# Kernel optimization log

Measured on AMD Instinct MI355X. Metric: run time of the kernel, lower is better.

The kernel has to match this reference:

```python
import jax, jax.numpy as jnp
import numpy as np


def setup_inputs() -> dict:
    key = jax.random.key(0)
    k1, k2 = jax.random.split(key)
    B, La, Lb, D = 32, 512, 512, 768
    a_bar = jax.random.normal(k1, (B, La, D), dtype=jnp.float32)
    b_bar = jax.random.normal(k2, (B, Lb, D), dtype=jnp.float32)
    return {"a_bar": a_bar, "b_bar": b_bar}


def reference(a_bar, b_bar):
    # e: [B, La, Lb] cross-attention scores
    e = jnp.einsum('bad,bcd->bac', a_bar, b_bar)
    # attend over b positions (softmax dim=2) -> aligned representation of a
    a_tilde = jnp.einsum('bac,bcd->bad', jax.nn.softmax(e, axis=2), b_bar)
    # attend over a positions (softmax dim=1), transpose, bmm with a_bar
    b_tilde = jnp.einsum('bac,bad->bcd', jax.nn.softmax(e, axis=1), a_bar)
    m_a = jnp.concatenate([a_bar, a_tilde, a_bar - a_tilde, a_bar * a_tilde], axis=-1)
    m_b = jnp.concatenate([b_bar, b_tilde, b_bar - b_tilde, b_bar * b_tilde], axis=-1)
    return (m_a, m_b)
```

## Files before the change

kernel.cpp:

```cpp
#include <hip/hip_runtime.h>
#include <hip/hip_bf16.h>
#include <math.h>

#define NB 32
#define LA 512
#define LB 512
#define DD 768

typedef __bf16 bf16x4 __attribute__((ext_vector_type(4)));
typedef __bf16 bf16x8 __attribute__((ext_vector_type(8)));
typedef float f32x4 __attribute__((ext_vector_type(4)));

#define LSTR 40

__device__ __forceinline__ void gload_lds16(const void* g, void* l) {
  __builtin_amdgcn_global_load_lds(
      (const __attribute__((address_space(1))) unsigned int*)g,
      (__attribute__((address_space(3))) unsigned int*)l, 16, 0, 0);
}

__global__ __launch_bounds__(256) void convert_kernel(
    const float* __restrict__ A, const float* __restrict__ B,
    __bf16* __restrict__ Ah, __bf16* __restrict__ Al,
    __bf16* __restrict__ Bh, __bf16* __restrict__ Bl,
    __bf16* __restrict__ AhT, __bf16* __restrict__ BhT) {
  const int zb = blockIdx.z;
  const int b = zb & (NB - 1);
  const bool isB = zb >= NB;
  const float* src = (isB ? B : A) + (size_t)b * 512 * DD;
  __bf16* H = (isB ? Bh : Ah) + (size_t)b * 512 * DD;
  __bf16* L = (isB ? Bl : Al) + (size_t)b * 512 * DD;
  __bf16* T = (isB ? BhT : AhT) + (size_t)b * DD * 512;
  const int d0 = blockIdx.x * 64, i0 = blockIdx.y * 64;
  __shared__ __bf16 Tt[64][72];
  const int t = threadIdx.x;
  const int c4 = t & 15, r = t >> 4;
#pragma unroll
  for (int p = 0; p < 4; ++p) {
    const int i = i0 + r + p * 16;
    const float4 v = *(const float4*)(src + (size_t)i * DD + d0 + c4 * 4);
    float vv[4] = {v.x, v.y, v.z, v.w};
    bf16x4 h, l;
#pragma unroll
    for (int q = 0; q < 4; ++q) {
      h[q] = (__bf16)vv[q];
      l[q] = (__bf16)(vv[q] - (float)h[q]);
    }
    *(bf16x4*)(H + (size_t)i * DD + d0 + c4 * 4) = h;
    *(bf16x4*)(L + (size_t)i * DD + d0 + c4 * 4) = l;
#pragma unroll
    for (int q = 0; q < 4; ++q) Tt[c4 * 4 + q][r + p * 16] = h[q];
  }
  __syncthreads();
  const int cc = t & 7, rr = t >> 3;
#pragma unroll
  for (int p = 0; p < 2; ++p) {
    const int d = d0 + rr + p * 32;
    *(bf16x8*)(T + (size_t)d * 512 + i0 + cc * 8) =
        *(bf16x8*)&Tt[rr + p * 32][cc * 8];
  }
}

__global__ __launch_bounds__(256) void gemm_e_mfma(
    const __bf16* __restrict__ Ah, const __bf16* __restrict__ Al,
    const __bf16* __restrict__ Bh, const __bf16* __restrict__ Bl,
    float* __restrict__ E) {
  __shared__ __bf16 AhS[128][32], AlS[128][32], BhS[128][32], BlS[128][32];

  const int b = blockIdx.z;
  const int i0 = blockIdx.x * 128, j0 = blockIdx.y * 128;
  const __bf16* AhB = Ah + (size_t)b * LA * DD;
  const __bf16* AlB = Al + (size_t)b * LA * DD;
  const __bf16* BhB = Bh + (size_t)b * LB * DD;
  const __bf16* BlB = Bl + (size_t)b * LB * DD;
  float* Eb = E + (size_t)b * LA * LB;

  const int t = threadIdx.x;
  const int lane = t & 63, wave = t >> 6;
  const int wm = (wave >> 1) * 64, wn = (wave & 1) * 64;
  const int quad = lane >> 4, l16 = lane & 15;
  const int lrow = lane >> 2, lcol = (lane & 3) * 8;

  f32x4 acc[4][4] = {};

  for (int k0 = 0; k0 < DD; k0 += 32) {
    __syncthreads();
#pragma unroll
    for (int n = 0; n < 2; ++n) {
      const int c = n * 4 + wave;
      const int row = c * 16 + lrow;
      const size_t gA = (size_t)(i0 + row) * DD + k0 + lcol;
      const size_t gB = (size_t)(j0 + row) * DD + k0 + lcol;
      gload_lds16(AhB + gA, (char*)&AhS[0][0] + c * 1024);
      gload_lds16(AlB + gA, (char*)&AlS[0][0] + c * 1024);
      gload_lds16(BhB + gB, (char*)&BhS[0][0] + c * 1024);
      gload_lds16(BlB + gB, (char*)&BlS[0][0] + c * 1024);
    }
    __syncthreads();

    bf16x8 fah[4], fal[4], fbh[4], fbl[4];
#pragma unroll
    for (int f = 0; f < 4; ++f) {
      fah[f] = *(bf16x8*)&AhS[wm + f * 16 + l16][quad * 8];
      fal[f] = *(bf16x8*)&AlS[wm + f * 16 + l16][quad * 8];
      fbh[f] = *(bf16x8*)&BhS[wn + f * 16 + l16][quad * 8];
      fbl[f] = *(bf16x8*)&BlS[wn + f * 16 + l16][quad * 8];
    }
#pragma unroll
    for (int fm = 0; fm < 4; ++fm)
#pragma unroll
      for (int fn = 0; fn < 4; ++fn) {
        acc[fm][fn] = __builtin_amdgcn_mfma_f32_16x16x32_bf16(fah[fm], fbh[fn], acc[fm][fn], 0, 0, 0);
        acc[fm][fn] = __builtin_amdgcn_mfma_f32_16x16x32_bf16(fah[fm], fbl[fn], acc[fm][fn], 0, 0, 0);
        acc[fm][fn] = __builtin_amdgcn_mfma_f32_16x16x32_bf16(fal[fm], fbh[fn], acc[fm][fn], 0, 0, 0);
      }
  }

#pragma unroll
  for (int fm = 0; fm < 4; ++fm)
#pragma unroll
    for (int r = 0; r < 4; ++r) {
      const int i = i0 + wm + fm * 16 + quad * 4 + r;
#pragma unroll
      for (int fn = 0; fn < 4; ++fn)
        Eb[(size_t)i * LB + j0 + wn + fn * 16 + l16] = acc[fm][fn][r];
    }
}

__global__ __launch_bounds__(256) void row_stats_kernel(
    const float* __restrict__ E, float* __restrict__ rmax,
    float* __restrict__ rsum) {
  const int wave = threadIdx.x >> 6;
  const int lane = threadIdx.x & 63;
  const int row = blockIdx.x * 4 + wave;
  const float* Er = E + (size_t)row * LB;
  float vals[8];
  float m = -INFINITY;
#pragma unroll
  for (int c = 0; c < 8; ++c) {
    vals[c] = Er[lane + c * 64];
    m = fmaxf(m, vals[c]);
  }
#pragma unroll
  for (int off = 32; off > 0; off >>= 1) m = fmaxf(m, __shfl_xor(m, off));
  float s = 0.f;
#pragma unroll
  for (int c = 0; c < 8; ++c) s += __expf(vals[c] - m);
#pragma unroll
  for (int off = 32; off > 0; off >>= 1) s += __shfl_xor(s, off);
  if (lane == 0) { rmax[row] = m; rsum[row] = s; }
}

__global__ __launch_bounds__(256) void col_partial(
    const float* __restrict__ E, float* __restrict__ pcm,
    float* __restrict__ pcs) {
  const int c = blockIdx.x * 256 + threadIdx.x;
  const int b = c >> 9, j = c & (LB - 1);
  const int i0 = blockIdx.y * 64;
  const float* Ep = E + ((size_t)b * LA + i0) * LB + j;
  float m = -INFINITY, s = 0.f;
#pragma unroll 4
  for (int i = 0; i < 64; ++i) {
    const float v = Ep[(size_t)i * LB];
    const float mn = fmaxf(m, v);
    s = s * __expf(m - mn) + __expf(v - mn);
    m = mn;
  }
  pcm[blockIdx.y * (NB * LB) + c] = m;
  pcs[blockIdx.y * (NB * LB) + c] = s;
}

__global__ __launch_bounds__(256) void col_combine(
    const float* __restrict__ pcm, const float* __restrict__ pcs,
    float* __restrict__ cmax, float* __restrict__ csum) {
  const int c = blockIdx.x * 256 + threadIdx.x;
  float m = -INFINITY, s = 0.f;
#pragma unroll
  for (int p = 0; p < 8; ++p) {
    const float mp = pcm[p * (NB * LB) + c];
    const float sp = pcs[p * (NB * LB) + c];
    const float mn = fmaxf(m, mp);
    s = s * __expf(m - mn) + sp * __expf(mp - mn);
    m = mn;
  }
  cmax[c] = m;
  csum[c] = s;
}

__global__ __launch_bounds__(256) void gemm_at_mfma(
    const float* __restrict__ E, const __bf16* __restrict__ BhT,
    const float* __restrict__ A, const float* __restrict__ rmax,
    const float* __restrict__ rsum, float* __restrict__ Ma) {
  __shared__ __bf16 Ps[128][LSTR];
  __shared__ __bf16 Bs[128][32];
  __shared__ float rm_s[128], rs_s[128];

  const int b = blockIdx.z;
  const int i0 = blockIdx.x * 128, d0 = blockIdx.y * 128;
  const float* Eb = E + (size_t)b * LA * LB;
  const __bf16* Tb = BhT + (size_t)b * DD * LB;
  const float* Ab = A + (size_t)b * LA * DD;

  const int t = threadIdx.x;
  const int lane = t & 63, wave = t >> 6;
  const int wm = (wave >> 1) * 64, wn = (wave & 1) * 64;
  const int quad = lane >> 4, l16 = lane & 15;
  const int sr = t >> 3, sc = t & 7;
  const int lrow = lane >> 2, lcol = (lane & 3) * 8;

  if (t < 128) {
    rm_s[t] = rmax[b * LA + i0 + t];
    rs_s[t] = 1.f / rsum[b * LA + i0 + t];
  }
  __syncthreads();

  f32x4 acc[4][4] = {};

  for (int k0 = 0; k0 < LB; k0 += 32) {
    float4 ev[4];
#pragma unroll
    for (int p = 0; p < 4; ++p)
      ev[p] = *(const float4*)(Eb + (size_t)(i0 + sr + p * 32) * LB + k0 + sc * 4);
    __syncthreads();
#pragma unroll
    for (int n = 0; n < 2; ++n) {
      const int c = n * 4 + wave;
      gload_lds16(Tb + (size_t)(d0 + c * 16 + lrow) * LB + k0 + lcol,
                  (char*)&Bs[0][0] + c * 1024);
    }
#pragma unroll
    for (int p = 0; p < 4; ++p) {
      const int m = sr + p * 32;
      const float rmv = rm_s[m], rsv = rs_s[m];
      float v[4] = {ev[p].x, ev[p].y, ev[p].z, ev[p].w};
      bf16x4 pb;
#pragma unroll
      for (int q = 0; q < 4; ++q) pb[q] = (__bf16)(__expf(v[q] - rmv) * rsv);
      *(bf16x4*)&Ps[m][sc * 4] = pb;
    }
    __syncthreads();

    bf16x8 fa[4], fb[4];
#pragma unroll
    for (int f = 0; f < 4; ++f) {
      fa[f] = *(bf16x8*)&Ps[wm + f * 16 + l16][quad * 8];
      fb[f] = *(bf16x8*)&Bs[wn + f * 16 + l16][quad * 8];
    }
#pragma unroll
    for (int fm = 0; fm < 4; ++fm)
#pragma unroll
      for (int fn = 0; fn < 4; ++fn)
        acc[fm][fn] = __builtin_amdgcn_mfma_f32_16x16x32_bf16(fa[fm], fb[fn], acc[fm][fn], 0, 0, 0);
  }

#pragma unroll
  for (int fm = 0; fm < 4; ++fm)
#pragma unroll
    for (int r = 0; r < 4; ++r) {
      const int i = i0 + wm + fm * 16 + quad * 4 + r;
      float* base = Ma + ((size_t)b * LA + i) * (4 * DD);
#pragma unroll
      for (int fn = 0; fn < 4; ++fn) {
        const int d = d0 + wn + fn * 16 + l16;
        const float av = Ab[(size_t)i * DD + d];
        const float at = acc[fm][fn][r];
        base[d] = av;
        base[DD + d] = at;
        base[2 * DD + d] = av - at;
        base[3 * DD + d] = av * at;
      }
    }
}

__global__ __launch_bounds__(256) void gemm_bt_mfma(
    const float* __restrict__ E, const __bf16* __restrict__ AhT,
    const float* __restrict__ Bm, const float* __restrict__ cmax,
    const float* __restrict__ csum, float* __restrict__ Mb) {
  __shared__ __bf16 Ps[128][LSTR];
  __shared__ __bf16 As[128][32];
  __shared__ float cm_s[128], cs_s[128];

  const int b = blockIdx.z;
  const int j0 = blockIdx.x * 128, d0 = blockIdx.y * 128;
  const float* Eb = E + (size_t)b * LA * LB;
  const __bf16* Tb = AhT + (size_t)b * DD * LA;
  const float* Bb = Bm + (size_t)b * LB * DD;

  const int t = threadIdx.x;
  const int lane = t & 63, wave = t >> 6;
  const int wm = (wave >> 1) * 64, wn = (wave & 1) * 64;
  const int quad = lane >> 4, l16 = lane & 15;
  const int ir = t >> 3, ic = t & 7;
  const int lrow = lane >> 2, lcol = (lane & 3) * 8;

  if (t < 128) {
    cm_s[t] = cmax[b * LB + j0 + t];
    cs_s[t] = 1.f / csum[b * LB + j0 + t];
  }
  __syncthreads();

  f32x4 acc[4][4] = {};

  for (int k0 = 0; k0 < LA; k0 += 32) {
    float4 ev[4];
#pragma unroll
    for (int p = 0; p < 4; ++p)
      ev[p] = *(const float4*)(Eb + (size_t)(k0 + ir) * LB + j0 + p * 32 + ic * 4);
    __syncthreads();
#pragma unroll
    for (int n = 0; n < 2; ++n) {
      const int c = n * 4 + wave;
      gload_lds16(Tb + (size_t)(d0 + c * 16 + lrow) * LA + k0 + lcol,
                  (char*)&As[0][0] + c * 1024);
    }
#pragma unroll
    for (int p = 0; p < 4; ++p) {
      const float4 cm4 = *(const float4*)&cm_s[p * 32 + ic * 4];
      const float4 cs4 = *(const float4*)&cs_s[p * 32 + ic * 4];
      float v[4] = {ev[p].x, ev[p].y, ev[p].z, ev[p].w};
      float cmv[4] = {cm4.x, cm4.y, cm4.z, cm4.w};
      float csv[4] = {cs4.x, cs4.y, cs4.z, cs4.w};
#pragma unroll
      for (int q = 0; q < 4; ++q)
        Ps[p * 32 + ic * 4 + q][ir] = (__bf16)(__expf(v[q] - cmv[q]) * csv[q]);
    }
    __syncthreads();

    bf16x8 fa[4], fb[4];
#pragma unroll
    for (int f = 0; f < 4; ++f) {
      fa[f] = *(bf16x8*)&Ps[wm + f * 16 + l16][quad * 8];
      fb[f] = *(bf16x8*)&As[wn + f * 16 + l16][quad * 8];
    }
#pragma unroll
    for (int fm = 0; fm < 4; ++fm)
#pragma unroll
      for (int fn = 0; fn < 4; ++fn)
        acc[fm][fn] = __builtin_amdgcn_mfma_f32_16x16x32_bf16(fa[fm], fb[fn], acc[fm][fn], 0, 0, 0);
  }

#pragma unroll
  for (int fm = 0; fm < 4; ++fm)
#pragma unroll
    for (int r = 0; r < 4; ++r) {
      const int j = j0 + wm + fm * 16 + quad * 4 + r;
      float* base = Mb + ((size_t)b * LB + j) * (4 * DD);
#pragma unroll
      for (int fn = 0; fn < 4; ++fn) {
        const int d = d0 + wn + fn * 16 + l16;
        const float bvv = Bb[(size_t)j * DD + d];
        const float bt = acc[fm][fn][r];
        base[d] = bvv;
        base[DD + d] = bt;
        base[2 * DD + d] = bvv - bt;
        base[3 * DD + d] = bvv * bt;
      }
    }
}

extern "C" void kernel_launch(void* const* d_in, const int* in_sizes, int n_in,
                              void* d_out, int out_size, void* d_ws,
                              size_t ws_size, hipStream_t stream) {
  const float* a = (const float*)d_in[0];
  const float* bb = (const float*)d_in[1];
  float* out = (float*)d_out;
  float* Ma = out;
  float* Mb = out + (size_t)NB * LA * 4 * DD;

  char* p = (char*)d_ws;
  float* E = (float*)p;      p += (size_t)NB * LA * LB * 4;
  float* rmax = (float*)p;   p += (size_t)NB * LA * 4;
  float* rsum = (float*)p;   p += (size_t)NB * LA * 4;
  float* cmax = (float*)p;   p += (size_t)NB * LB * 4;
  float* csum = (float*)p;   p += (size_t)NB * LB * 4;
  float* pcm = (float*)p;    p += (size_t)8 * NB * LB * 4;
  float* pcs = (float*)p;    p += (size_t)8 * NB * LB * 4;
  __bf16* Ah = (__bf16*)p;   p += (size_t)NB * LA * DD * 2;
  __bf16* Al = (__bf16*)p;   p += (size_t)NB * LA * DD * 2;
  __bf16* Bh = (__bf16*)p;   p += (size_t)NB * LB * DD * 2;
  __bf16* Bl = (__bf16*)p;   p += (size_t)NB * LB * DD * 2;
  __bf16* AhT = (__bf16*)p;  p += (size_t)NB * DD * LA * 2;
  __bf16* BhT = (__bf16*)p;  p += (size_t)NB * DD * LB * 2;

  convert_kernel<<<dim3(DD / 64, 512 / 64, 2 * NB), 256, 0, stream>>>(
      a, bb, Ah, Al, Bh, Bl, AhT, BhT);
  gemm_e_mfma<<<dim3(LA / 128, LB / 128, NB), 256, 0, stream>>>(Ah, Al, Bh, Bl, E);
  row_stats_kernel<<<dim3(NB * LA / 4), 256, 0, stream>>>(E, rmax, rsum);
  col_partial<<<dim3(NB * LB / 256, 8), 256, 0, stream>>>(E, pcm, pcs);
  col_combine<<<dim3(NB * LB / 256), 256, 0, stream>>>(pcm, pcs, cmax, csum);
  gemm_at_mfma<<<dim3(LA / 128, DD / 128, NB), 256, 0, stream>>>(E, BhT, a, rmax,
                                                                 rsum, Ma);
  gemm_bt_mfma<<<dim3(LB / 128, DD / 128, NB), 256, 0, stream>>>(E, AhT, bb, cmax,
                                                                 csum, Mb);
}
```

Baseline: 685.3 us.

## Double-buffer LDS in the three GEMMs and remap blocks by XCD per batch

Each of the three MFMA GEMM kernels now keeps two LDS buffers. The next K-tile (global_load_lds, plus the E loads and softmax writes in the attention GEMMs) is issued while MFMAs run on the current tile, and each iteration needs one barrier instead of two. The grids are flattened to 1D and block ids are remapped so that all tiles of one batch land on the same XCD (id&7 striding), which is meant to improve L2 reuse of E and the operands. The cost is double the LDS per block, which can reduce occupancy, and more live registers for the prefetched E values.

```diff
diff --git a/kernel.cpp b/kernel.cpp
--- a/kernel.cpp
+++ b/kernel.cpp
@@ -65,10 +65,13 @@
     const __bf16* __restrict__ Ah, const __bf16* __restrict__ Al,
     const __bf16* __restrict__ Bh, const __bf16* __restrict__ Bl,
     float* __restrict__ E) {
-  __shared__ __bf16 AhS[128][32], AlS[128][32], BhS[128][32], BlS[128][32];
-
-  const int b = blockIdx.z;
-  const int i0 = blockIdx.x * 128, j0 = blockIdx.y * 128;
+  __shared__ __bf16 S[2][4][128][32];
+
+  const int id = blockIdx.x;
+  const int wg = (id & 7) * 64 + (id >> 3);
+  const int b = wg >> 4, tl = wg & 15;
+  const int i0 = (tl & 3) * 128, j0 = (tl >> 2) * 128;
+
   const __bf16* AhB = Ah + (size_t)b * LA * DD;
   const __bf16* AlB = Al + (size_t)b * LA * DD;
   const __bf16* BhB = Bh + (size_t)b * LB * DD;
@@ -81,30 +84,36 @@
   const int quad = lane >> 4, l16 = lane & 15;
   const int lrow = lane >> 2, lcol = (lane & 3) * 8;
 
-  f32x4 acc[4][4] = {};
-
-  for (int k0 = 0; k0 < DD; k0 += 32) {
-    __syncthreads();
+  auto stage = [&](int buf, int k0) {
 #pragma unroll
     for (int n = 0; n < 2; ++n) {
       const int c = n * 4 + wave;
       const int row = c * 16 + lrow;
       const size_t gA = (size_t)(i0 + row) * DD + k0 + lcol;
       const size_t gB = (size_t)(j0 + row) * DD + k0 + lcol;
-      gload_lds16(AhB + gA, (char*)&AhS[0][0] + c * 1024);
-      gload_lds16(AlB + gA, (char*)&AlS[0][0] + c * 1024);
-      gload_lds16(BhB + gB, (char*)&BhS[0][0] + c * 1024);
-      gload_lds16(BlB + gB, (char*)&BlS[0][0] + c * 1024);
-    }
-    __syncthreads();
+      char* base = (char*)&S[buf][0][0][0];
+      gload_lds16(AhB + gA, base + c * 1024);
+      gload_lds16(AlB + gA, base + 8192 + c * 1024);
+      gload_lds16(BhB + gB, base + 16384 + c * 1024);
+      gload_lds16(BlB + gB, base + 24576 + c * 1024);
+    }
+  };
+
+  f32x4 acc[4][4] = {};
+
+  stage(0, 0);
+  __syncthreads();
+  int cur = 0;
+  for (int k0 = 0; k0 < DD; k0 += 32) {
+    if (k0 + 32 < DD) stage(cur ^ 1, k0 + 32);
 
     bf16x8 fah[4], fal[4], fbh[4], fbl[4];
 #pragma unroll
     for (int f = 0; f < 4; ++f) {
-      fah[f] = *(bf16x8*)&AhS[wm + f * 16 + l16][quad * 8];
-      fal[f] = *(bf16x8*)&AlS[wm + f * 16 + l16][quad * 8];
-      fbh[f] = *(bf16x8*)&BhS[wn + f * 16 + l16][quad * 8];
-      fbl[f] = *(bf16x8*)&BlS[wn + f * 16 + l16][quad * 8];
+      fah[f] = *(bf16x8*)&S[cur][0][wm + f * 16 + l16][quad * 8];
+      fal[f] = *(bf16x8*)&S[cur][1][wm + f * 16 + l16][quad * 8];
+      fbh[f] = *(bf16x8*)&S[cur][2][wn + f * 16 + l16][quad * 8];
+      fbl[f] = *(bf16x8*)&S[cur][3][wn + f * 16 + l16][quad * 8];
     }
 #pragma unroll
     for (int fm = 0; fm < 4; ++fm)
@@ -114,6 +123,8 @@
         acc[fm][fn] = __builtin_amdgcn_mfma_f32_16x16x32_bf16(fah[fm], fbl[fn], acc[fm][fn], 0, 0, 0);
         acc[fm][fn] = __builtin_amdgcn_mfma_f32_16x16x32_bf16(fal[fm], fbh[fn], acc[fm][fn], 0, 0, 0);
       }
+    __syncthreads();
+    cur ^= 1;
   }
 
 #pragma unroll
@@ -191,12 +202,15 @@
     const float* __restrict__ E, const __bf16* __restrict__ BhT,
     const float* __restrict__ A, const float* __restrict__ rmax,
     const float* __restrict__ rsum, float* __restrict__ Ma) {
-  __shared__ __bf16 Ps[128][LSTR];
-  __shared__ __bf16 Bs[128][32];
+  __shared__ __bf16 Ps[2][128][LSTR];
+  __shared__ __bf16 Bs[2][128][32];
   __shared__ float rm_s[128], rs_s[128];
 
-  const int b = blockIdx.z;
-  const int i0 = blockIdx.x * 128, d0 = blockIdx.y * 128;
+  const int id = blockIdx.x;
+  const int wg = (id & 7) * 96 + (id >> 3);
+  const int b = wg / 24, r24 = wg % 24;
+  const int i0 = (r24 / 6) * 128, d0 = (r24 % 6) * 128;
+
   const float* Eb = E + (size_t)b * LA * LB;
   const __bf16* Tb = BhT + (size_t)b * DD * LB;
   const float* Ab = A + (size_t)b * LA * DD;
@@ -214,20 +228,20 @@
   }
   __syncthreads();
 
-  f32x4 acc[4][4] = {};
-
-  for (int k0 = 0; k0 < LB; k0 += 32) {
-    float4 ev[4];
+  auto loadE = [&](int k0, float4* ev) {
 #pragma unroll
     for (int p = 0; p < 4; ++p)
       ev[p] = *(const float4*)(Eb + (size_t)(i0 + sr + p * 32) * LB + k0 + sc * 4);
-    __syncthreads();
+  };
+  auto stageB = [&](int buf, int k0) {
 #pragma unroll
     for (int n = 0; n < 2; ++n) {
       const int c = n * 4 + wave;
       gload_lds16(Tb + (size_t)(d0 + c * 16 + lrow) * LB + k0 + lcol,
-                  (char*)&Bs[0][0] + c * 1024);
-    }
+                  (char*)&Bs[buf][0][0] + c * 1024);
+    }
+  };
+  auto writeP = [&](int buf, const float4* ev) {
 #pragma unroll
     for (int p = 0; p < 4; ++p) {
       const int m = sr + p * 32;
@@ -236,21 +250,38 @@
       bf16x4 pb;
 #pragma unroll
       for (int q = 0; q < 4; ++q) pb[q] = (__bf16)(__expf(v[q] - rmv) * rsv);
-      *(bf16x4*)&Ps[m][sc * 4] = pb;
-    }
-    __syncthreads();
+      *(bf16x4*)&Ps[buf][m][sc * 4] = pb;
+    }
+  };
+
+  f32x4 acc[4][4] = {};
+
+  float4 ev[4];
+  loadE(0, ev);
+  stageB(0, 0);
+  writeP(0, ev);
+  __syncthreads();
+  int cur = 0;
+  for (int k0 = 0; k0 < LB; k0 += 32) {
+    const bool nxt = (k0 + 32 < LB);
+    float4 evn[4];
+    if (nxt) { loadE(k0 + 32, evn); stageB(cur ^ 1, k0 + 32); }
 
     bf16x8 fa[4], fb[4];
 #pragma unroll
     for (int f = 0; f < 4; ++f) {
-      fa[f] = *(bf16x8*)&Ps[wm + f * 16 + l16][quad * 8];
-      fb[f] = *(bf16x8*)&Bs[wn + f * 16 + l16][quad * 8];
+      fa[f] = *(bf16x8*)&Ps[cur][wm + f * 16 + l16][quad * 8];
+      fb[f] = *(bf16x8*)&Bs[cur][wn + f * 16 + l16][quad * 8];
     }
 #pragma unroll
     for (int fm = 0; fm < 4; ++fm)
 #pragma unroll
       for (int fn = 0; fn < 4; ++fn)
         acc[fm][fn] = __builtin_amdgcn_mfma_f32_16x16x32_bf16(fa[fm], fb[fn], acc[fm][fn], 0, 0, 0);
+
+    if (nxt) writeP(cur ^ 1, evn);
+    __syncthreads();
+    cur ^= 1;
   }
 
 #pragma unroll
@@ -276,12 +307,15 @@
     const float* __restrict__ E, const __bf16* __restrict__ AhT,
     const float* __restrict__ Bm, const float* __restrict__ cmax,
     const float* __restrict__ csum, float* __restrict__ Mb) {
-  __shared__ __bf16 Ps[128][LSTR];
-  __shared__ __bf16 As[128][32];
+  __shared__ __bf16 Ps[2][128][LSTR];
+  __shared__ __bf16 As[2][128][32];
   __shared__ float cm_s[128], cs_s[128];
 
-  const int b = blockIdx.z;
-  const int j0 = blockIdx.x * 128, d0 = blockIdx.y * 128;
+  const int id = blockIdx.x;
+  const int wg = (id & 7) * 96 + (id >> 3);
+  const int b = wg / 24, r24 = wg % 24;
+  const int j0 = (r24 / 6) * 128, d0 = (r24 % 6) * 128;
+
   const float* Eb = E + (size_t)b * LA * LB;
   const __bf16* Tb = AhT + (size_t)b * DD * LA;
   const float* Bb = Bm + (size_t)b * LB * DD;
@@ -299,20 +333,20 @@
   }
   __syncthreads();
 
-  f32x4 acc[4][4] = {};
-
-  for (int k0 = 0; k0 < LA; k0 += 32) {
-    float4 ev[4];
+  auto loadE = [&](int k0, float4* ev) {
 #pragma unroll
     for (int p = 0; p < 4; ++p)
       ev[p] = *(const float4*)(Eb + (size_t)(k0 + ir) * LB + j0 + p * 32 + ic * 4);
-    __syncthreads();
+  };
+  auto stageA = [&](int buf, int k0) {
 #pragma unroll
     for (int n = 0; n < 2; ++n) {
       const int c = n * 4 + wave;
       gload_lds16(Tb + (size_t)(d0 + c * 16 + lrow) * LA + k0 + lcol,
-                  (char*)&As[0][0] + c * 1024);
-    }
+                  (char*)&As[buf][0][0] + c * 1024);
+    }
+  };
+  auto writeP = [&](int buf, const float4* ev) {
 #pragma unroll
     for (int p = 0; p < 4; ++p) {
       const float4 cm4 = *(const float4*)&cm_s[p * 32 + ic * 4];
@@ -322,21 +356,38 @@
       float csv[4] = {cs4.x, cs4.y, cs4.z, cs4.w};
 #pragma unroll
       for (int q = 0; q < 4; ++q)
-        Ps[p * 32 + ic * 4 + q][ir] = (__bf16)(__expf(v[q] - cmv[q]) * csv[q]);
-    }
-    __syncthreads();
+        Ps[buf][p * 32 + ic * 4 + q][ir] = (__bf16)(__expf(v[q] - cmv[q]) * csv[q]);
+    }
+  };
+
+  f32x4 acc[4][4] = {};
+
+  float4 ev[4];
+  loadE(0, ev);
+  stageA(0, 0);
+  writeP(0, ev);
+  __syncthreads();
+  int cur = 0;
+  for (int k0 = 0; k0 < LA; k0 += 32) {
+    const bool nxt = (k0 + 32 < LA);
+    float4 evn[4];
+    if (nxt) { loadE(k0 + 32, evn); stageA(cur ^ 1, k0 + 32); }
 
     bf16x8 fa[4], fb[4];
 #pragma unroll
     for (int f = 0; f < 4; ++f) {
-      fa[f] = *(bf16x8*)&Ps[wm + f * 16 + l16][quad * 8];
-      fb[f] = *(bf16x8*)&As[wn + f * 16 + l16][quad * 8];
+      fa[f] = *(bf16x8*)&Ps[cur][wm + f * 16 + l16][quad * 8];
+      fb[f] = *(bf16x8*)&As[cur][wn + f * 16 + l16][quad * 8];
     }
 #pragma unroll
     for (int fm = 0; fm < 4; ++fm)
 #pragma unroll
       for (int fn = 0; fn < 4; ++fn)
         acc[fm][fn] = __builtin_amdgcn_mfma_f32_16x16x32_bf16(fa[fm], fb[fn], acc[fm][fn], 0, 0, 0);
+
+    if (nxt) writeP(cur ^ 1, evn);
+    __syncthreads();
+    cur ^= 1;
   }
 
 #pragma unroll
@@ -384,12 +435,10 @@
 
   convert_kernel<<<dim3(DD / 64, 512 / 64, 2 * NB), 256, 0, stream>>>(
       a, bb, Ah, Al, Bh, Bl, AhT, BhT);
-  gemm_e_mfma<<<dim3(LA / 128, LB / 128, NB), 256, 0, stream>>>(Ah, Al, Bh, Bl, E);
+  gemm_e_mfma<<<dim3(512), 256, 0, stream>>>(Ah, Al, Bh, Bl, E);
   row_stats_kernel<<<dim3(NB * LA / 4), 256, 0, stream>>>(E, rmax, rsum);
   col_partial<<<dim3(NB * LB / 256, 8), 256, 0, stream>>>(E, pcm, pcs);
   col_combine<<<dim3(NB * LB / 256), 256, 0, stream>>>(pcm, pcs, cmax, csum);
-  gemm_at_mfma<<<dim3(LA / 128, DD / 128, NB), 256, 0, stream>>>(E, BhT, a, rmax,
-                                                                 rsum, Ma);
-  gemm_bt_mfma<<<dim3(LB / 128, DD / 128, NB), 256, 0, stream>>>(E, AhT, bb, cmax,
-                                                                 csum, Mb);
-}
+  gemm_at_mfma<<<dim3(768), 256, 0, stream>>>(E, BhT, a, rmax, rsum, Ma);
+  gemm_bt_mfma<<<dim3(768), 256, 0, stream>>>(E, AhT, bb, cmax, csum, Mb);
+}
```

Result: no change. 684.2 us (-0.2%).
